# Kernel optimization log

Measured on AMD Instinct MI355X. Metric: run time of the kernel, lower is better.

## Reference

```python
import jax, jax.numpy as jnp
import numpy as np

N_NODES = 100000
N_EDGES = 1000000
D_FEAT = 128


def setup_inputs() -> dict:
    key = jax.random.key(0)
    kx, ks, kd = jax.random.split(key, 3)
    x = jax.random.normal(kx, (N_NODES, D_FEAT), dtype=jnp.float32)
    src = jax.random.randint(ks, (N_EDGES,), 0, N_NODES, dtype=jnp.int64)
    dst = jax.random.randint(kd, (N_EDGES,), 0, N_NODES, dtype=jnp.int64)
    return {"x": x, "src": src, "dst": dst}


def reference(x, src, dst):
    # DGL u_dot_v: per-edge dot product of source and destination node features.
    # Gather [E, D] twice, reduce over D -> score shape [E, 1] (matches DGL).
    score = jnp.einsum("ed,ed->e", x[src], x[dst])
    return score[:, None]
```

## Files before the change

### kernel.cpp

```cpp
#include <hip/hip_runtime.h>
#include <hip/hip_bf16.h>
#include <hip/hip_fp16.h>


#define D_FEAT 128

typedef _Float16 half8 __attribute__((ext_vector_type(8)));

__global__ __launch_bounds__(256)
void cvt_f32_to_f16(const float* __restrict__ x,
                    _Float16* __restrict__ xh,
                    int n) {
    int i = blockIdx.x * blockDim.x + threadIdx.x;
    int base = i * 8;
    if (base >= n) return;
    const float4* xv = reinterpret_cast<const float4*>(x);
    float4 v0 = xv[i * 2];
    float4 v1 = xv[i * 2 + 1];
    half8 h;
    h[0] = (_Float16)v0.x; h[1] = (_Float16)v0.y;
    h[2] = (_Float16)v0.z; h[3] = (_Float16)v0.w;
    h[4] = (_Float16)v1.x; h[5] = (_Float16)v1.y;
    h[6] = (_Float16)v1.z; h[7] = (_Float16)v1.w;
    reinterpret_cast<half8*>(xh)[i] = h;
}

__global__ __launch_bounds__(256)
void u_dot_v_f16(const _Float16* __restrict__ xh,
                 const int* __restrict__ src,
                 const int* __restrict__ dst,
                 float* __restrict__ out,
                 int n_edges) {
    int gtid = blockIdx.x * blockDim.x + threadIdx.x;
    int edge = gtid >> 3;
    int lane = gtid & 7;
    if (edge >= n_edges) return;

    int s = src[edge];
    int d = dst[edge];

    const half8* xs = reinterpret_cast<const half8*>(xh + (size_t)s * D_FEAT);
    const half8* xd = reinterpret_cast<const half8*>(xh + (size_t)d * D_FEAT);

    half8 a0 = xs[lane];
    half8 a1 = xs[lane + 8];
    half8 b0 = xd[lane];
    half8 b1 = xd[lane + 8];

    float sum = 0.0f;
    #pragma unroll
    for (int k = 0; k < 8; ++k)
        sum += (float)a0[k] * (float)b0[k] + (float)a1[k] * (float)b1[k];

    #pragma unroll
    for (int off = 4; off > 0; off >>= 1)
        sum += __shfl_xor(sum, off, 64);

    if (lane == 0) out[edge] = sum;
}

__global__ __launch_bounds__(256)
void u_dot_v_f32(const float* __restrict__ x,
                 const int* __restrict__ src,
                 const int* __restrict__ dst,
                 float* __restrict__ out,
                 int n_edges) {
    int gtid = blockIdx.x * blockDim.x + threadIdx.x;
    int edge = gtid >> 3;
    int lane = gtid & 7;
    if (edge >= n_edges) return;

    int s = src[edge];
    int d = dst[edge];

    const float4* xs = reinterpret_cast<const float4*>(x + (size_t)s * D_FEAT);
    const float4* xd = reinterpret_cast<const float4*>(x + (size_t)d * D_FEAT);

    float4 a0 = xs[lane];
    float4 a1 = xs[lane + 8];
    float4 a2 = xs[lane + 16];
    float4 a3 = xs[lane + 24];
    float4 b0 = xd[lane];
    float4 b1 = xd[lane + 8];
    float4 b2 = xd[lane + 16];
    float4 b3 = xd[lane + 24];

    float sum = a0.x * b0.x + a0.y * b0.y + a0.z * b0.z + a0.w * b0.w
              + a1.x * b1.x + a1.y * b1.y + a1.z * b1.z + a1.w * b1.w
              + a2.x * b2.x + a2.y * b2.y + a2.z * b2.z + a2.w * b2.w
              + a3.x * b3.x + a3.y * b3.y + a3.z * b3.z + a3.w * b3.w;

    #pragma unroll
    for (int off = 4; off > 0; off >>= 1)
        sum += __shfl_xor(sum, off, 64);

    if (lane == 0) out[edge] = sum;
}

extern "C" void kernel_launch(void* const* d_in, const int* in_sizes, int n_in,
                              void* d_out, int out_size, void* d_ws, size_t ws_size,
                              hipStream_t stream) {
    const float* x   = (const float*)d_in[0];
    const int*   src = (const int*)d_in[1];
    const int*   dst = (const int*)d_in[2];
    float*       out = (float*)d_out;

    int n_x     = in_sizes[0];
    int n_edges = in_sizes[1];

    size_t need = (size_t)n_x * sizeof(_Float16);

    if (ws_size >= need && (n_x % 8) == 0) {
        _Float16* xh = (_Float16*)d_ws;

        int cvt_threads = 256;
        int cvt_items   = n_x / 8;
        int cvt_blocks  = (cvt_items + cvt_threads - 1) / cvt_threads;
        cvt_f32_to_f16<<<cvt_blocks, cvt_threads, 0, stream>>>(x, xh, n_x);

        int threads = 256;
        long long total = (long long)n_edges * 8;
        int blocks = (int)((total + threads - 1) / threads);
        u_dot_v_f16<<<blocks, threads, 0, stream>>>(xh, src, dst, out, n_edges);
    } else {
        int threads = 256;
        long long total = (long long)n_edges * 8;
        int blocks = (int)((total + threads - 1) / threads);
        u_dot_v_f32<<<blocks, threads, 0, stream>>>(x, src, dst, out, n_edges);
    }
}
```

Before: 149.2 us.

## Split feature dim into slices to gather per-slice with cache-resident tables

Converts x to fp16 in a sliced layout (8 slices of 16 features, each slice a contiguous [nodes,16] table of about 3.2MB) so that each gather pass touches only one small table that can stay resident in cache. Each slice pass writes per-edge partial dot products to a workspace buffer, and a final kernel sums the 8 partials per edge. The intent is to turn random HBM row gathers into cache hits. The cost is reading src/dst 8 times, writing and re-reading 32MB of partials, and launching an extra kernel.

```diff
diff --git a/kernel.cpp b/kernel.cpp
--- a/kernel.cpp
+++ b/kernel.cpp
@@ -3,20 +3,94 @@
 #include <hip/hip_fp16.h>
 
 
-#define D_FEAT 128
+#define D_FEAT   128
+#define N_SLICES 8
+#define SLICE_F  16
 
-typedef _Float16 half8 __attribute__((ext_vector_type(8)));
+typedef _Float16 half8  __attribute__((ext_vector_type(8)));
+typedef _Float16 half16 __attribute__((ext_vector_type(16)));
 
 __global__ __launch_bounds__(256)
-void cvt_f32_to_f16(const float* __restrict__ x,
-                    _Float16* __restrict__ xh,
-                    int n) {
+void cvt_slice(const float* __restrict__ x,
+               _Float16* __restrict__ xh,
+               int n_nodes) {
+    int node = blockIdx.x * blockDim.x + threadIdx.x;
+    int s = blockIdx.y;
+    if (node >= n_nodes) return;
+    const float4* srcv =
+        reinterpret_cast<const float4*>(x + (size_t)node * D_FEAT + s * SLICE_F);
+    float4 v0 = srcv[0], v1 = srcv[1], v2 = srcv[2], v3 = srcv[3];
+    half16 h;
+    h[0] = (_Float16)v0.x;  h[1] = (_Float16)v0.y;
+    h[2] = (_Float16)v0.z;  h[3] = (_Float16)v0.w;
+    h[4] = (_Float16)v1.x;  h[5] = (_Float16)v1.y;
+    h[6] = (_Float16)v1.z;  h[7] = (_Float16)v1.w;
+    h[8] = (_Float16)v2.x;  h[9] = (_Float16)v2.y;
+    h[10] = (_Float16)v2.z; h[11] = (_Float16)v2.w;
+    h[12] = (_Float16)v3.x; h[13] = (_Float16)v3.y;
+    h[14] = (_Float16)v3.z; h[15] = (_Float16)v3.w;
+    *reinterpret_cast<half16*>(xh + ((size_t)s * n_nodes + node) * SLICE_F) = h;
+}
+
+__global__ __launch_bounds__(256)
+void gather_slice(const _Float16* __restrict__ xh,
+                  const int* __restrict__ src,
+                  const int* __restrict__ dst,
+                  float* __restrict__ partial,
+                  int n_nodes, int n_edges) {
+    int s = blockIdx.x & 7;
+    int e = (blockIdx.x >> 3) * 256 + threadIdx.x;
+    if (e >= n_edges) return;
+
+    int a = src[e];
+    int b = dst[e];
+
+    const half8* pa =
+        reinterpret_cast<const half8*>(xh + ((size_t)s * n_nodes + a) * SLICE_F);
+    const half8* pb =
+        reinterpret_cast<const half8*>(xh + ((size_t)s * n_nodes + b) * SLICE_F);
+    half8 a0 = pa[0], a1 = pa[1];
+    half8 b0 = pb[0], b1 = pb[1];
+
+    float sum = 0.0f;
+    #pragma unroll
+    for (int k = 0; k < 8; ++k)
+        sum += (float)a0[k] * (float)b0[k] + (float)a1[k] * (float)b1[k];
+
+    partial[(size_t)s * n_edges + e] = sum;
+}
+
+__global__ __launch_bounds__(256)
+void reduce_slices(const float* __restrict__ partial,
+                   float* __restrict__ out,
+                   int n_edges) {
     int i = blockIdx.x * blockDim.x + threadIdx.x;
-    int base = i * 8;
-    if (base >= n) return;
+    int e = i * 4;
+    if (e + 3 < n_edges) {
+        float4 acc = make_float4(0.f, 0.f, 0.f, 0.f);
+        #pragma unroll
+        for (int s = 0; s < N_SLICES; ++s) {
+            float4 p = *reinterpret_cast<const float4*>(partial + (size_t)s * n_edges + e);
+            acc.x += p.x; acc.y += p.y; acc.z += p.z; acc.w += p.w;
+        }
+        *reinterpret_cast<float4*>(out + e) = acc;
+    } else if (e < n_edges) {
+        for (; e < n_edges; ++e) {
+            float acc = 0.f;
+            #pragma unroll
+            for (int s = 0; s < N_SLICES; ++s)
+                acc += partial[(size_t)s * n_edges + e];
+            out[e] = acc;
+        }
+    }
+}
+
+__global__ __launch_bounds__(256)
+void cvt_f32_to_f16(const float* __restrict__ x, _Float16* __restrict__ xh, int n) {
+    int i = blockIdx.x * blockDim.x + threadIdx.x;
+    if (i * 8 >= n) return;
     const float4* xv = reinterpret_cast<const float4*>(x);
-    float4 v0 = xv[i * 2];
-    float4 v1 = xv[i * 2 + 1];
+    float4 v0 = xv[i * 2], v1 = xv[i * 2 + 1];
     half8 h;
     h[0] = (_Float16)v0.x; h[1] = (_Float16)v0.y;
     h[2] = (_Float16)v0.z; h[3] = (_Float16)v0.w;
@@ -26,74 +100,46 @@
 }
 
 __global__ __launch_bounds__(256)
-void u_dot_v_f16(const _Float16* __restrict__ xh,
-                 const int* __restrict__ src,
-                 const int* __restrict__ dst,
-                 float* __restrict__ out,
-                 int n_edges) {
+void u_dot_v_f16(const _Float16* __restrict__ xh, const int* __restrict__ src,
+                 const int* __restrict__ dst, float* __restrict__ out, int n_edges) {
     int gtid = blockIdx.x * blockDim.x + threadIdx.x;
     int edge = gtid >> 3;
     int lane = gtid & 7;
     if (edge >= n_edges) return;
-
-    int s = src[edge];
-    int d = dst[edge];
-
+    int s = src[edge], d = dst[edge];
     const half8* xs = reinterpret_cast<const half8*>(xh + (size_t)s * D_FEAT);
     const half8* xd = reinterpret_cast<const half8*>(xh + (size_t)d * D_FEAT);
-
-    half8 a0 = xs[lane];
-    half8 a1 = xs[lane + 8];
-    half8 b0 = xd[lane];
-    half8 b1 = xd[lane + 8];
-
+    half8 a0 = xs[lane], a1 = xs[lane + 8];
+    half8 b0 = xd[lane], b1 = xd[lane + 8];
     float sum = 0.0f;
     #pragma unroll
     for (int k = 0; k < 8; ++k)
         sum += (float)a0[k] * (float)b0[k] + (float)a1[k] * (float)b1[k];
-
     #pragma unroll
     for (int off = 4; off > 0; off >>= 1)
         sum += __shfl_xor(sum, off, 64);
-
     if (lane == 0) out[edge] = sum;
 }
 
 __global__ __launch_bounds__(256)
-void u_dot_v_f32(const float* __restrict__ x,
-                 const int* __restrict__ src,
-                 const int* __restrict__ dst,
-                 float* __restrict__ out,
-                 int n_edges) {
+void u_dot_v_f32(const float* __restrict__ x, const int* __restrict__ src,
+                 const int* __restrict__ dst, float* __restrict__ out, int n_edges) {
     int gtid = blockIdx.x * blockDim.x + threadIdx.x;
     int edge = gtid >> 3;
     int lane = gtid & 7;
     if (edge >= n_edges) return;
-
-    int s = src[edge];
-    int d = dst[edge];
-
+    int s = src[edge], d = dst[edge];
     const float4* xs = reinterpret_cast<const float4*>(x + (size_t)s * D_FEAT);
     const float4* xd = reinterpret_cast<const float4*>(x + (size_t)d * D_FEAT);
-
-    float4 a0 = xs[lane];
-    float4 a1 = xs[lane + 8];
-    float4 a2 = xs[lane + 16];
-    float4 a3 = xs[lane + 24];
-    float4 b0 = xd[lane];
-    float4 b1 = xd[lane + 8];
-    float4 b2 = xd[lane + 16];
-    float4 b3 = xd[lane + 24];
-
+    float4 a0 = xs[lane], a1 = xs[lane + 8], a2 = xs[lane + 16], a3 = xs[lane + 24];
+    float4 b0 = xd[lane], b1 = xd[lane + 8], b2 = xd[lane + 16], b3 = xd[lane + 24];
     float sum = a0.x * b0.x + a0.y * b0.y + a0.z * b0.z + a0.w * b0.w
               + a1.x * b1.x + a1.y * b1.y + a1.z * b1.z + a1.w * b1.w
               + a2.x * b2.x + a2.y * b2.y + a2.z * b2.z + a2.w * b2.w
               + a3.x * b3.x + a3.y * b3.y + a3.z * b3.z + a3.w * b3.w;
-
     #pragma unroll
     for (int off = 4; off > 0; off >>= 1)
         sum += __shfl_xor(sum, off, 64);
-
     if (lane == 0) out[edge] = sum;
 }
 
@@ -107,25 +153,34 @@
 
     int n_x     = in_sizes[0];
     int n_edges = in_sizes[1];
+    int n_nodes = n_x / D_FEAT;
 
-    size_t need = (size_t)n_x * sizeof(_Float16);
+    size_t xh_bytes   = (size_t)n_x * sizeof(_Float16);
+    size_t part_bytes = (size_t)N_SLICES * n_edges * sizeof(float);
 
-    if (ws_size >= need && (n_x % 8) == 0) {
+    if (ws_size >= xh_bytes + part_bytes) {
+        _Float16* xh      = (_Float16*)d_ws;
+        float*    partial = (float*)((char*)d_ws + xh_bytes);
+
+        dim3 cgrid((n_nodes + 255) / 256, N_SLICES);
+        cvt_slice<<<cgrid, 256, 0, stream>>>(x, xh, n_nodes);
+
+        int chunks = (n_edges + 255) / 256;
+        gather_slice<<<chunks * N_SLICES, 256, 0, stream>>>(
+            xh, src, dst, partial, n_nodes, n_edges);
+
+        int items = (n_edges + 3) / 4;
+        reduce_slices<<<(items + 255) / 256, 256, 0, stream>>>(partial, out, n_edges);
+    } else if (ws_size >= xh_bytes && (n_x % 8) == 0) {
         _Float16* xh = (_Float16*)d_ws;
-
-        int cvt_threads = 256;
-        int cvt_items   = n_x / 8;
-        int cvt_blocks  = (cvt_items + cvt_threads - 1) / cvt_threads;
-        cvt_f32_to_f16<<<cvt_blocks, cvt_threads, 0, stream>>>(x, xh, n_x);
-
-        int threads = 256;
+        int cvt_blocks = (n_x / 8 + 255) / 256;
+        cvt_f32_to_f16<<<cvt_blocks, 256, 0, stream>>>(x, xh, n_x);
         long long total = (long long)n_edges * 8;
-        int blocks = (int)((total + threads - 1) / threads);
-        u_dot_v_f16<<<blocks, threads, 0, stream>>>(xh, src, dst, out, n_edges);
+        u_dot_v_f16<<<(int)((total + 255) / 256), 256, 0, stream>>>(
+            xh, src, dst, out, n_edges);
     } else {
-        int threads = 256;
         long long total = (long long)n_edges * 8;
-        int blocks = (int)((total + threads - 1) / threads);
-        u_dot_v_f32<<<blocks, threads, 0, stream>>>(x, src, dst, out, n_edges);
+        u_dot_v_f32<<<(int)((total + 255) / 256), 256, 0, stream>>>(
+            x, src, dst, out, n_edges);
     }
 }
```

Result: slower. 192.6 us (+29.1%).
